# Optimization experiments

Hardware: AMD Instinct MI355X
Metric: run time of the kernel (lower is better)

The kernel has to match this reference:

```python
import jax, jax.numpy as jnp
import numpy as np

B, CIN, H, W = 4, 128, 160, 160
K = 100          # num instances
CH = 8           # mask head channels
OUT = 8          # mask branch out channels
STRIDE = 4
EPS = 1e-5


def conv3x3(x, w):
    # x: [B,C,H,W], w: [O,C,3,3] -> [B,O,H,W], stride 1, pad 1
    return jax.lax.conv_general_dilated(x, w, (1, 1), 'SAME',
                                        dimension_numbers=('NCHW', 'OIHW', 'NCHW'))


def setup_inputs() -> dict:
    key = jax.random.key(0)
    ks = jax.random.split(key, 6)
    cnn_feature = jax.random.normal(ks[0], (B, CIN, H, W), jnp.float32)
    tower_w = jax.random.normal(ks[1], (4, 128, 128, 3, 3), jnp.float32) * 0.03
    bn_gamma = jnp.ones((4, 128), jnp.float32)
    bn_beta = jnp.zeros((4, 128), jnp.float32)
    bn_mean = jnp.zeros((4, 128), jnp.float32)
    bn_var = jnp.ones((4, 128), jnp.float32)
    proj_w = jax.random.normal(ks[2], (OUT, 128), jnp.float32) * 0.05
    proj_b = jnp.zeros((OUT,), jnp.float32)
    ctrl_w = jax.random.normal(ks[3], (169, CIN, 3, 3), jnp.float32) * 0.01
    ctrl_b = jnp.zeros((169,), jnp.float32)
    detection = jax.random.randint(ks[4], (K, 2), 0, min(H, W), dtype=jnp.int32)
    return dict(cnn_feature=cnn_feature, tower_w=tower_w, bn_gamma=bn_gamma,
                bn_beta=bn_beta, bn_mean=bn_mean, bn_var=bn_var,
                proj_w=proj_w, proj_b=proj_b, ctrl_w=ctrl_w, ctrl_b=ctrl_b,
                detection=detection)


def reference(cnn_feature, tower_w, bn_gamma, bn_beta, bn_mean, bn_var,
              proj_w, proj_b, ctrl_w, ctrl_b, detection):
    x = cnn_feature
    for i in range(4):
        x = conv3x3(x, tower_w[i])
        inv = bn_gamma[i] / jnp.sqrt(bn_var[i] + EPS)            # [128]
        shift = bn_beta[i] - bn_mean[i] * inv
        x = jax.nn.relu(x * inv[None, :, None, None] + shift[None, :, None, None])
    mask_feats = jnp.einsum('bchw,oc->bohw', x, proj_w) + proj_b[None, :, None, None]

    # ----- controller: 3x3 conv producing 169 dynamic params per pixel -----
    ctrl = conv3x3(cnn_feature, ctrl_w) + ctrl_b[None, :, None, None]  # [B,169,H,W]

    # ----- gather per-instance params at detection centers (im_inds all 0) -----
    xs = detection[:, 0]
    ys = detection[:, 1]
    params = ctrl[0][:, ys, xs].T  # [K,169]

    # ----- relative coordinates -----
    sx = jnp.arange(W, dtype=jnp.float32) * STRIDE + STRIDE // 2
    sy = jnp.arange(H, dtype=jnp.float32) * STRIDE + STRIDE // 2
    gy, gx = jnp.meshgrid(sy, sx, indexing='ij')
    locations = jnp.stack([gx.reshape(-1), gy.reshape(-1)], axis=1)   # [HW,2]
    ct = detection.astype(jnp.float32) * STRIDE                        # [K,2]
    rel = (ct[:, None, :] - locations[None, :, :]).transpose(0, 2, 1)  # [K,2,HW]

    feats = jnp.broadcast_to(mask_feats[0].reshape(1, OUT, H * W), (K, OUT, H * W))
    h = jnp.concatenate([rel, feats], axis=1)  # [K,10,HW]

    # ----- parse dynamic params: weights first, then biases -----
    w0 = params[:, 0:80].reshape(K, CH, OUT + 2)     # (8+2)*8
    w1 = params[:, 80:144].reshape(K, CH, CH)        # 8*8
    w2 = params[:, 144:152].reshape(K, 1, CH)        # 8*1
    b0 = params[:, 152:160]
    b1 = params[:, 160:168]
    b2 = params[:, 168:169]

    # ----- dynamic grouped 1x1 convs == per-instance matmuls -----
    h = jax.nn.relu(jnp.einsum('koc,kcp->kop', w0, h) + b0[:, :, None])
    h = jax.nn.relu(jnp.einsum('koc,kcp->kop', w1, h) + b1[:, :, None])
    h = jnp.einsum('koc,kcp->kop', w2, h) + b2[:, :, None]  # [K,1,HW]
    return h.reshape(K, H, W)
```

## Files before the change

kernel.cpp:

```cpp
#include <hip/hip_runtime.h>
#include <hip/hip_bf16.h>

#define H 160
#define W 160
#define HW 25600
#define ROWB 40960

typedef __attribute__((ext_vector_type(8))) short bf16x8;
typedef __attribute__((ext_vector_type(4))) float f32x4;
typedef __attribute__((ext_vector_type(8))) unsigned short ushort8v;
typedef __attribute__((ext_vector_type(4))) unsigned short ushort4v;

typedef __attribute__((address_space(1))) const unsigned int gu32;
typedef __attribute__((address_space(3))) unsigned int lu32;

__device__ __forceinline__ void gload16(const void* g, void* l) {
    __builtin_amdgcn_global_load_lds((gu32*)g, (lu32*)l, 16, 0, 0);
}

__device__ __forceinline__ unsigned short f2b(float f) {
    unsigned int u = __float_as_uint(f);
    unsigned int r = (u + 0x7fffu + ((u >> 16) & 1u)) >> 16;
    return (unsigned short)r;
}
__device__ __forceinline__ float b2f(unsigned short b) {
    return __uint_as_float(((unsigned int)b) << 16);
}

#define LGKM0() asm volatile("s_waitcnt lgkmcnt(0)" ::: "memory")
#define BARRIER() asm volatile("s_barrier" ::: "memory")


__global__ __launch_bounds__(256) void fused_prep(
    const float* __restrict__ cnn,
    const float* __restrict__ tw,
    const float* __restrict__ gamma, const float* __restrict__ beta,
    const float* __restrict__ mean,  const float* __restrict__ var,
    const float* __restrict__ cw, const float* __restrict__ cb,
    const int*   __restrict__ det,
    char* __restrict__ actX, char* __restrict__ wbf,
    float* __restrict__ invshift, float* __restrict__ params)
{
    const int tid = threadIdx.x;
    const int b = blockIdx.x;

    if (b < 100) {
        __shared__ float patch[1152];
        const int k = b;
        const int xk = det[2 * k];
        const int yk = det[2 * k + 1];
        for (int i = tid; i < 1152; i += 256) {
            int ci = i / 9;
            int rem = i - ci * 9;
            int r = rem / 3, s = rem - r * 3;
            int gy = yk + r - 1, gx = xk + s - 1;
            float v = 0.f;
            if ((unsigned)gy < (unsigned)H && (unsigned)gx < (unsigned)W)
                v = cnn[ci * HW + gy * W + gx];
            patch[i] = v;
        }
        __syncthreads();
        if (tid < 169) {
            const float4* cw4 = (const float4*)&cw[tid * 1152];
            const float4* p4  = (const float4*)patch;
            float a0 = 0.f, a1 = 0.f, a2 = 0.f, a3 = 0.f;
            for (int i = 0; i < 288; i += 4) {
                float4 pa = p4[i],     wa = cw4[i];
                float4 pb_ = p4[i+1],  wb_ = cw4[i+1];
                float4 pc = p4[i+2],   wc_ = cw4[i+2];
                float4 pd = p4[i+3],   wd = cw4[i+3];
                a0 += pa.x*wa.x + pa.y*wa.y + pa.z*wa.z + pa.w*wa.w;
                a1 += pb_.x*wb_.x + pb_.y*wb_.y + pb_.z*wb_.z + pb_.w*wb_.w;
                a2 += pc.x*wc_.x + pc.y*wc_.y + pc.z*wc_.z + pc.w*wc_.w;
                a3 += pd.x*wd.x + pd.y*wd.y + pd.z*wd.z + pd.w*wd.w;
            }
            params[k * 169 + tid] = cb[tid] + ((a0 + a1) + (a2 + a3));
        }
    } else if (b < 300) {
        int blk = b - 100;
        int p0  = blk * 128 + (tid & 31) * 4;
        int cbh = tid >> 5;
#pragma unroll
        for (int pass = 0; pass < 2; ++pass) {
            int cb2 = pass * 8 + cbh;
            int ci0 = cb2 * 8;
            ushort8v o0, o1, o2, o3;
#pragma unroll
            for (int jj = 0; jj < 8; ++jj) {
                float4 v = *(const float4*)&cnn[(ci0 + jj) * HW + p0];
                o0[jj] = f2b(v.x);
                o1[jj] = f2b(v.y);
                o2[jj] = f2b(v.z);
                o3[jj] = f2b(v.w);
            }
            *(ushort8v*)(actX + (p0 + 0) * 256 + ((cb2 ^ ((p0 + 0) & 15)) * 16)) = o0;
            *(ushort8v*)(actX + (p0 + 1) * 256 + ((cb2 ^ ((p0 + 1) & 15)) * 16)) = o1;
            *(ushort8v*)(actX + (p0 + 2) * 256 + ((cb2 ^ ((p0 + 2) & 15)) * 16)) = o2;
            *(ushort8v*)(actX + (p0 + 3) * 256 + ((cb2 ^ ((p0 + 3) & 15)) * 16)) = o3;
        }
    } else {
        int idx = (b - 300) * 256 + tid;
        int ci = idx & 127;
        int co = (idx >> 7) & 127;
        int l  = idx >> 14;
        int kk = ci >> 5;
        int cw2 = ci & 31;
        const float* src = tw + ((l * 128 + co) * 128 + ci) * 9;
        char* dst = wbf + l * 294912 + kk * 8192 + co * 64 + cw2 * 2;
#pragma unroll
        for (int t = 0; t < 9; ++t)
            *(unsigned short*)(dst + t * 32768) = f2b(src[t]);

        if (b == 300) {
            for (int c = tid; c < 512; c += 256) {
                int ll = c >> 7, ch = c & 127;
                float inv = gamma[ll * 128 + ch] * rsqrtf(var[ll * 128 + ch] + 1e-5f);
                float sh  = beta[ll * 128 + ch] - mean[ll * 128 + ch] * inv;
                invshift[ll * 256 + ch] = inv;
                invshift[ll * 256 + 128 + ch] = sh;
            }
        }
    }
}

template <int PROJ>
__global__ __launch_bounds__(512, 1) void conv_mfma(
    const char* __restrict__ actin,
    const char* __restrict__ wpl,
    const float* __restrict__ invshift_l,
    char* __restrict__ actout,
    const float* __restrict__ pw,
    const float* __restrict__ pb,
    float* __restrict__ mf)
{
    __shared__ __align__(16) char smem[78848];
    char* IT = smem;
    char* WQ = smem + 46080;

    const int tid  = threadIdx.x;
    const int lane = tid & 63;
    const int w    = tid >> 6;
    const int wp   = w >> 1;
    const int wc   = w & 1;
    const int g    = lane >> 4;
    const int i15  = lane & 15;

    const int bx = blockIdx.x;
    const int by = blockIdx.y;
    const int tx0 = bx * 16 - 1;
    const int ty0 = by * 8 - 1;

    for (int it = 0; it < 6; ++it) {
        int c = it * 512 + tid;
        if (c < 2880) {
            int row  = c / 288;
            int rem  = c - row * 288;
            int px_i = rem >> 4;
            int bo   = (rem & 15) * 16;
            int cy = min(max(ty0 + row, 0), H - 1);
            int cx = min(max(tx0 + px_i, 0), W - 1);
            char* ldsb = IT + (it * 512 + (tid & ~63)) * 16;
            gload16(actin + cy * ROWB + cx * 256 + bo, ldsb);
        }
    }
#pragma unroll
    for (int pl = 0; pl < 3; ++pl)
        gload16(wpl + pl * 8192 + tid * 16,
                WQ + pl * 8192 + (tid & ~63) * 16);
    asm volatile("s_waitcnt vmcnt(2)" ::: "memory");
    for (int c = tid; c < 2880; c += 512) {
        int row  = c / 288;
        int rem  = c - row * 288;
        int px_i = rem >> 4;
        int gy = ty0 + row, gx = tx0 + px_i;
        if ((unsigned)gy >= (unsigned)H || (unsigned)gx >= (unsigned)W) {
            f32x4 z = {0.f, 0.f, 0.f, 0.f};
            *(f32x4*)(IT + c * 16) = z;
        }
    }
    LGKM0();
    BARRIER();

    f32x4 acc[4][2];
#pragma unroll
    for (int cf = 0; cf < 4; ++cf)
#pragma unroll
        for (int pf = 0; pf < 2; ++pf)
            acc[cf][pf] = (f32x4){0.f, 0.f, 0.f, 0.f};

#define CSTAGE(J, WN) {                                                        \
    if ((J) <= 32)                                                             \
        gload16(wpl + ((J) + 3) * 8192 + tid * 16,                             \
                WQ + (((J) + 3) & 3) * 8192 + (tid & ~63) * 16);               \
    asm volatile("s_waitcnt vmcnt(" #WN ")" ::: "memory");                     \
    {                                                                          \
        const int tap = (J) >> 2, kk = (J) & 3;                                \
        const int r = tap / 3, s = tap - r * 3;                                \
        const char* wbse = WQ + ((J) & 3) * 8192 + (wc * 64 + i15) * 64 + g * 16; \
        bf16x8 a0 = *(const bf16x8*)(wbse + 0 * 1024);                         \
        bf16x8 a1 = *(const bf16x8*)(wbse + 1 * 1024);                         \
        bf16x8 a2 = *(const bf16x8*)(wbse + 2 * 1024);                         \
        bf16x8 a3 = *(const bf16x8*)(wbse + 3 * 1024);                         \
        const int slotb = ((kk * 4 + g) ^ ((i15 + s + 15) & 15)) * 16;         \
        const char* ib = IT + (i15 + s) * 256 + slotb;                         \
        bf16x8 b0 = *(const bf16x8*)(ib + (wp * 2 + 0 + r) * 4608);            \
        bf16x8 b1 = *(const bf16x8*)(ib + (wp * 2 + 1 + r) * 4608);            \
        acc[0][0] = __builtin_amdgcn_mfma_f32_16x16x32_bf16(a0, b0, acc[0][0], 0, 0, 0); \
        acc[0][1] = __builtin_amdgcn_mfma_f32_16x16x32_bf16(a0, b1, acc[0][1], 0, 0, 0); \
        acc[1][0] = __builtin_amdgcn_mfma_f32_16x16x32_bf16(a1, b0, acc[1][0], 0, 0, 0); \
        acc[1][1] = __builtin_amdgcn_mfma_f32_16x16x32_bf16(a1, b1, acc[1][1], 0, 0, 0); \
        acc[2][0] = __builtin_amdgcn_mfma_f32_16x16x32_bf16(a2, b0, acc[2][0], 0, 0, 0); \
        acc[2][1] = __builtin_amdgcn_mfma_f32_16x16x32_bf16(a2, b1, acc[2][1], 0, 0, 0); \
        acc[3][0] = __builtin_amdgcn_mfma_f32_16x16x32_bf16(a3, b0, acc[3][0], 0, 0, 0); \
        acc[3][1] = __builtin_amdgcn_mfma_f32_16x16x32_bf16(a3, b1, acc[3][1], 0, 0, 0); \
    }                                                                          \
    BARRIER();                                                                 \
}

    CSTAGE(0,2)  CSTAGE(1,2)  CSTAGE(2,2)  CSTAGE(3,2)  CSTAGE(4,2)  CSTAGE(5,2)
    CSTAGE(6,2)  CSTAGE(7,2)  CSTAGE(8,2)  CSTAGE(9,2)  CSTAGE(10,2) CSTAGE(11,2)
    CSTAGE(12,2) CSTAGE(13,2) CSTAGE(14,2) CSTAGE(15,2) CSTAGE(16,2) CSTAGE(17,2)
    CSTAGE(18,2) CSTAGE(19,2) CSTAGE(20,2) CSTAGE(21,2) CSTAGE(22,2) CSTAGE(23,2)
    CSTAGE(24,2) CSTAGE(25,2) CSTAGE(26,2) CSTAGE(27,2) CSTAGE(28,2) CSTAGE(29,2)
    CSTAGE(30,2) CSTAGE(31,2) CSTAGE(32,2) CSTAGE(33,1) CSTAGE(34,0) CSTAGE(35,0)
#undef CSTAGE

    if (PROJ == 0) {
        const int gx = bx * 16 + i15;
#pragma unroll
        for (int cf = 0; cf < 4; ++cf) {
            int co0 = wc * 64 + cf * 16 + g * 4;
            int cbx = wc * 8 + cf * 2 + (g >> 1);
            int sbyte = ((cbx ^ i15) * 16) + (g & 1) * 8;
            f32x4 inv4 = *(const f32x4*)&invshift_l[co0];
            f32x4 sh4  = *(const f32x4*)&invshift_l[128 + co0];
#pragma unroll
            for (int pf = 0; pf < 2; ++pf) {
                int gy = by * 8 + wp * 2 + pf;
                f32x4 v = acc[cf][pf];
                ushort4v o;
                o.x = f2b(fmaxf(v.x * inv4.x + sh4.x, 0.f));
                o.y = f2b(fmaxf(v.y * inv4.y + sh4.y, 0.f));
                o.z = f2b(fmaxf(v.z * inv4.z + sh4.z, 0.f));
                o.w = f2b(fmaxf(v.w * inv4.w + sh4.w, 0.f));
                *(ushort4v*)(actout + gy * ROWB + gx * 256 + sbyte) = o;
            }
        }
    } else {
        char* actF = smem;
        float* spw = (float*)(smem + 32768);
        __syncthreads();
#pragma unroll
        for (int cf = 0; cf < 4; ++cf) {
            int co0 = wc * 64 + cf * 16 + g * 4;
            int cbx = wc * 8 + cf * 2 + (g >> 1);
            int sbyte = ((cbx ^ i15) * 16) + (g & 1) * 8;
            f32x4 inv4 = *(const f32x4*)&invshift_l[co0];
            f32x4 sh4  = *(const f32x4*)&invshift_l[128 + co0];
#pragma unroll
            for (int pf = 0; pf < 2; ++pf) {
                int px = (wp * 2 + pf) * 16 + i15;
                f32x4 v = acc[cf][pf];
                ushort4v o;
                o.x = f2b(fmaxf(v.x * inv4.x + sh4.x, 0.f));
                o.y = f2b(fmaxf(v.y * inv4.y + sh4.y, 0.f));
                o.z = f2b(fmaxf(v.z * inv4.z + sh4.z, 0.f));
                o.w = f2b(fmaxf(v.w * inv4.w + sh4.w, 0.f));
                *(ushort4v*)(actF + px * 256 + sbyte) = o;
            }
        }
        for (int i = tid; i < 1024; i += 512) spw[i] = pw[i];
        __syncthreads();
        int pxt = tid >> 2;
        int o0  = (tid & 3) * 2;
        float s0 = 0.f, s1 = 0.f;
#pragma unroll
        for (int cb2 = 0; cb2 < 16; ++cb2) {
            ushort8v vv = *(const ushort8v*)(actF + pxt * 256 + ((cb2 ^ (pxt & 15)) * 16));
#pragma unroll
            for (int j = 0; j < 8; ++j) {
                float f = b2f(vv[j]);
                int ci = cb2 * 8 + j;
                s0 += f * spw[o0 * 128 + ci];
                s1 += f * spw[(o0 + 1) * 128 + ci];
            }
        }
        int p = (by * 8 + (pxt >> 4)) * W + bx * 16 + (pxt & 15);
        mf[o0 * HW + p]       = s0 + pb[o0];
        mf[(o0 + 1) * HW + p] = s1 + pb[o0 + 1];
    }
}

__global__ __launch_bounds__(256) void head_kernel(
    const float* __restrict__ mf, const float* __restrict__ params,
    const int* __restrict__ det, float* __restrict__ out)
{
    __shared__ float sp[1690];
    __shared__ int sdet[20];
    const int tid = threadIdx.x;
    const int kg = blockIdx.y;
    for (int i = tid; i < 1690; i += 256) sp[i] = params[kg * 1690 + i];
    if (tid < 20) sdet[tid] = det[kg * 20 + tid];
    __syncthreads();

    const int p = blockIdx.x * 256 + tid;
    const int x = p % W;
    const int y = p / W;
    const float fx = (float)(x * 4 + 2);
    const float fy = (float)(y * 4 + 2);

    float f[8];
#pragma unroll
    for (int o = 0; o < 8; ++o) f[o] = mf[o * HW + p];

#pragma unroll 2
    for (int j = 0; j < 10; ++j) {
        const float* spj = &sp[j * 169];
        const float rel0 = (float)(sdet[2 * j] * 4) - fx;
        const float rel1 = (float)(sdet[2 * j + 1] * 4) - fy;
        float h0[8];
#pragma unroll
        for (int o = 0; o < 8; ++o) {
            float a = spj[152 + o] + spj[o * 10] * rel0 + spj[o * 10 + 1] * rel1;
#pragma unroll
            for (int c = 0; c < 8; ++c) a += spj[o * 10 + 2 + c] * f[c];
            h0[o] = fmaxf(a, 0.f);
        }
        float h1[8];
#pragma unroll
        for (int o = 0; o < 8; ++o) {
            float a = spj[160 + o];
#pragma unroll
            for (int c = 0; c < 8; ++c) a += spj[80 + o * 8 + c] * h0[c];
            h1[o] = fmaxf(a, 0.f);
        }
        float r = spj[168];
#pragma unroll
        for (int c = 0; c < 8; ++c) r += spj[144 + c] * h1[c];
        out[(kg * 10 + j) * HW + p] = r;
    }
}

extern "C" void kernel_launch(void* const* d_in, const int* in_sizes, int n_in,
                              void* d_out, int out_size, void* d_ws, size_t ws_size,
                              hipStream_t stream)
{
    const float* cnn    = (const float*)d_in[0];
    const float* towerw = (const float*)d_in[1];
    const float* gamma  = (const float*)d_in[2];
    const float* beta   = (const float*)d_in[3];
    const float* meanp  = (const float*)d_in[4];
    const float* varp   = (const float*)d_in[5];
    const float* projw  = (const float*)d_in[6];
    const float* projb  = (const float*)d_in[7];
    const float* ctrlw  = (const float*)d_in[8];
    const float* ctrlb  = (const float*)d_in[9];
    const int*   det    = (const int*)d_in[10];
    float* out = (float*)d_out;

    char*  outb     = (char*)d_out;
    char*  X        = outb;
    char*  wbf      = outb + 6553600;
    float* invshift = (float*)(outb + 7733248);

    char*  Y      = (char*)d_ws;
    float* mf     = (float*)((char*)d_ws + 6553600);
    float* params = (float*)((char*)d_ws + 7372800);

    fused_prep<<<dim3(556), dim3(256), 0, stream>>>(
        cnn, towerw, gamma, beta, meanp, varp, ctrlw, ctrlb, det,
        X, wbf, invshift, params);

    const dim3 cgrid(10, 20);
    conv_mfma<0><<<cgrid, dim3(512), 0, stream>>>(X, wbf + 0 * 294912, invshift + 0 * 256,
                                                  Y, nullptr, nullptr, nullptr);
    conv_mfma<0><<<cgrid, dim3(512), 0, stream>>>(Y, wbf + 1 * 294912, invshift + 1 * 256,
                                                  X, nullptr, nullptr, nullptr);
    conv_mfma<0><<<cgrid, dim3(512), 0, stream>>>(X, wbf + 2 * 294912, invshift + 2 * 256,
                                                  Y, nullptr, nullptr, nullptr);
    conv_mfma<1><<<cgrid, dim3(512), 0, stream>>>(Y, wbf + 3 * 294912, invshift + 3 * 256,
                                                  nullptr, projw, projb, mf);

    head_kernel<<<dim3(100, 10), dim3(256), 0, stream>>>(mf, params, det, out);
}
```

Measured before the change: 120.1 us.

## Move controller param gather into first conv launch using transposed weights

The per-instance controller dot products move out of the prep kernel and run as 100 extra blocks of the first tower conv launch, so they can fill CUs idle beside the 200 conv blocks. The prep kernel now transposes the controller weights into a [1152][169] layout so threads read them coalesced. The conv grid becomes 1D with the block index decoded into x and y. The cost is an extra transpose pass and one accumulator per thread in place of four, which lengthens the dependent add chain in the dot product.

After: 130.4 us. 1.09x slower.

```diff
diff --git a/kernel.cpp b/kernel.cpp
--- a/kernel.cpp
+++ b/kernel.cpp
@@ -36,48 +36,15 @@
     const float* __restrict__ tw,
     const float* __restrict__ gamma, const float* __restrict__ beta,
     const float* __restrict__ mean,  const float* __restrict__ var,
-    const float* __restrict__ cw, const float* __restrict__ cb,
-    const int*   __restrict__ det,
+    const float* __restrict__ cw,
     char* __restrict__ actX, char* __restrict__ wbf,
-    float* __restrict__ invshift, float* __restrict__ params)
+    float* __restrict__ invshift, float* __restrict__ cwT)
 {
     const int tid = threadIdx.x;
     const int b = blockIdx.x;
 
-    if (b < 100) {
-        __shared__ float patch[1152];
-        const int k = b;
-        const int xk = det[2 * k];
-        const int yk = det[2 * k + 1];
-        for (int i = tid; i < 1152; i += 256) {
-            int ci = i / 9;
-            int rem = i - ci * 9;
-            int r = rem / 3, s = rem - r * 3;
-            int gy = yk + r - 1, gx = xk + s - 1;
-            float v = 0.f;
-            if ((unsigned)gy < (unsigned)H && (unsigned)gx < (unsigned)W)
-                v = cnn[ci * HW + gy * W + gx];
-            patch[i] = v;
-        }
-        __syncthreads();
-        if (tid < 169) {
-            const float4* cw4 = (const float4*)&cw[tid * 1152];
-            const float4* p4  = (const float4*)patch;
-            float a0 = 0.f, a1 = 0.f, a2 = 0.f, a3 = 0.f;
-            for (int i = 0; i < 288; i += 4) {
-                float4 pa = p4[i],     wa = cw4[i];
-                float4 pb_ = p4[i+1],  wb_ = cw4[i+1];
-                float4 pc = p4[i+2],   wc_ = cw4[i+2];
-                float4 pd = p4[i+3],   wd = cw4[i+3];
-                a0 += pa.x*wa.x + pa.y*wa.y + pa.z*wa.z + pa.w*wa.w;
-                a1 += pb_.x*wb_.x + pb_.y*wb_.y + pb_.z*wb_.z + pb_.w*wb_.w;
-                a2 += pc.x*wc_.x + pc.y*wc_.y + pc.z*wc_.z + pc.w*wc_.w;
-                a3 += pd.x*wd.x + pd.y*wd.y + pd.z*wd.z + pd.w*wd.w;
-            }
-            params[k * 169 + tid] = cb[tid] + ((a0 + a1) + (a2 + a3));
-        }
-    } else if (b < 300) {
-        int blk = b - 100;
+    if (b < 200) {
+        int blk = b;
         int p0  = blk * 128 + (tid & 31) * 4;
         int cbh = tid >> 5;
 #pragma unroll
@@ -98,8 +65,8 @@
             *(ushort8v*)(actX + (p0 + 2) * 256 + ((cb2 ^ ((p0 + 2) & 15)) * 16)) = o2;
             *(ushort8v*)(actX + (p0 + 3) * 256 + ((cb2 ^ ((p0 + 3) & 15)) * 16)) = o3;
         }
-    } else {
-        int idx = (b - 300) * 256 + tid;
+    } else if (b < 456) {
+        int idx = (b - 200) * 256 + tid;
         int ci = idx & 127;
         int co = (idx >> 7) & 127;
         int l  = idx >> 14;
@@ -111,7 +78,7 @@
         for (int t = 0; t < 9; ++t)
             *(unsigned short*)(dst + t * 32768) = f2b(src[t]);
 
-        if (b == 300) {
+        if (b == 200) {
             for (int c = tid; c < 512; c += 256) {
                 int ll = c >> 7, ch = c & 127;
                 float inv = gamma[ll * 128 + ch] * rsqrtf(var[ll * 128 + ch] + 1e-5f);
@@ -120,10 +87,17 @@
                 invshift[ll * 256 + 128 + ch] = sh;
             }
         }
-    }
-}
-
-template <int PROJ>
+    } else {
+        int idx = (b - 456) * 256 + tid;
+        if (idx < 194688) {
+            int j = idx / 169;
+            int o = idx - j * 169;
+            cwT[idx] = cw[o * 1152 + j];
+        }
+    }
+}
+
+template <int PROJ, int CTRL>
 __global__ __launch_bounds__(512, 1) void conv_mfma(
     const char* __restrict__ actin,
     const char* __restrict__ wpl,
@@ -131,13 +105,46 @@
     char* __restrict__ actout,
     const float* __restrict__ pw,
     const float* __restrict__ pb,
-    float* __restrict__ mf)
+    float* __restrict__ mf,
+    const float* __restrict__ cnn,
+    const float* __restrict__ cwT,
+    const float* __restrict__ cbp,
+    const int*   __restrict__ det,
+    float* __restrict__ params)
 {
     __shared__ __align__(16) char smem[78848];
+
+    const int tid  = threadIdx.x;
+
+    if (CTRL && blockIdx.x >= 200) {
+        float* patch = (float*)smem;
+        const int k = blockIdx.x - 200;
+        const int xk = det[2 * k];
+        const int yk = det[2 * k + 1];
+        for (int i = tid; i < 1152; i += 512) {
+            int ci = i / 9;
+            int rem = i - ci * 9;
+            int r = rem / 3, s = rem - r * 3;
+            int gy = yk + r - 1, gx = xk + s - 1;
+            float v = 0.f;
+            if ((unsigned)gy < (unsigned)H && (unsigned)gx < (unsigned)W)
+                v = cnn[ci * HW + gy * W + gx];
+            patch[i] = v;
+        }
+        __syncthreads();
+        if (tid < 169) {
+            float acc = 0.f;
+#pragma unroll 8
+            for (int j = 0; j < 1152; ++j)
+                acc += cwT[j * 169 + tid] * patch[j];
+            params[k * 169 + tid] = acc + cbp[tid];
+        }
+        return;
+    }
+
     char* IT = smem;
     char* WQ = smem + 46080;
 
-    const int tid  = threadIdx.x;
     const int lane = tid & 63;
     const int w    = tid >> 6;
     const int wp   = w >> 1;
@@ -145,8 +152,9 @@
     const int g    = lane >> 4;
     const int i15  = lane & 15;
 
-    const int bx = blockIdx.x;
-    const int by = blockIdx.y;
+    const int bb = blockIdx.x;
+    const int bx = bb % 10;
+    const int by = bb / 10;
     const int tx0 = bx * 16 - 1;
     const int ty0 = by * 8 - 1;
 
@@ -362,24 +370,32 @@
     char*  X        = outb;
     char*  wbf      = outb + 6553600;
     float* invshift = (float*)(outb + 7733248);
+    float* cwT      = (float*)(outb + 7737344);
 
     char*  Y      = (char*)d_ws;
     float* mf     = (float*)((char*)d_ws + 6553600);
     float* params = (float*)((char*)d_ws + 7372800);
 
-    fused_prep<<<dim3(556), dim3(256), 0, stream>>>(
-        cnn, towerw, gamma, beta, meanp, varp, ctrlw, ctrlb, det,
-        X, wbf, invshift, params);
-
-    const dim3 cgrid(10, 20);
-    conv_mfma<0><<<cgrid, dim3(512), 0, stream>>>(X, wbf + 0 * 294912, invshift + 0 * 256,
-                                                  Y, nullptr, nullptr, nullptr);
-    conv_mfma<0><<<cgrid, dim3(512), 0, stream>>>(Y, wbf + 1 * 294912, invshift + 1 * 256,
-                                                  X, nullptr, nullptr, nullptr);
-    conv_mfma<0><<<cgrid, dim3(512), 0, stream>>>(X, wbf + 2 * 294912, invshift + 2 * 256,
-                                                  Y, nullptr, nullptr, nullptr);
-    conv_mfma<1><<<cgrid, dim3(512), 0, stream>>>(Y, wbf + 3 * 294912, invshift + 3 * 256,
-                                                  nullptr, projw, projb, mf);
+    fused_prep<<<dim3(1217), dim3(256), 0, stream>>>(
+        cnn, towerw, gamma, beta, meanp, varp, ctrlw,
+        X, wbf, invshift, cwT);
+
+    conv_mfma<0, 1><<<dim3(300), dim3(512), 0, stream>>>(
+        X, wbf + 0 * 294912, invshift + 0 * 256, Y,
+        nullptr, nullptr, nullptr,
+        cnn, cwT, ctrlb, det, params);
+    conv_mfma<0, 0><<<dim3(200), dim3(512), 0, stream>>>(
+        Y, wbf + 1 * 294912, invshift + 1 * 256, X,
+        nullptr, nullptr, nullptr,
+        nullptr, nullptr, nullptr, nullptr, nullptr);
+    conv_mfma<0, 0><<<dim3(200), dim3(512), 0, stream>>>(
+        X, wbf + 2 * 294912, invshift + 2 * 256, Y,
+        nullptr, nullptr, nullptr,
+        nullptr, nullptr, nullptr, nullptr, nullptr);
+    conv_mfma<1, 0><<<dim3(200), dim3(512), 0, stream>>>(
+        Y, wbf + 3 * 294912, invshift + 3 * 256, nullptr,
+        projw, projb, mf,
+        nullptr, nullptr, nullptr, nullptr, nullptr);
 
     head_kernel<<<dim3(100, 10), dim3(256), 0, stream>>>(mf, params, det, out);
 }
```
